# Kernel tuning notes

Hardware: AMD Instinct MI355X
Metric: run time of the kernel (lower is better)

## Reference

```python
import jax, jax.numpy as jnp
import numpy as np

D = 256; NH = 8; NL = 4; NP = 4; HD = D // NH
SHAPES = np.array([[180, 180], [90, 90], [45, 45], [23, 23]], dtype=np.int32)
LQ = int((SHAPES[:, 0] * SHAPES[:, 1]).sum())  # 43054
STARTS = np.concatenate([[0], np.cumsum(SHAPES[:, 0] * SHAPES[:, 1])[:-1]]).astype(np.int32)


def setup_inputs():
    ks = jax.random.split(jax.random.key(0), 16)
    s = 0.02
    p = lambda k, shp: jax.random.normal(k, shp, jnp.float32) * s
    return {
        "query": jax.random.normal(ks[0], (1, LQ, D), jnp.float32),
        "ref_points": jax.random.uniform(ks[1], (1, LQ, NL, 2), dtype=jnp.float32),
        "pos": jax.random.normal(ks[2], (1, LQ, D), jnp.float32),
        "input_spatial_shapes": jnp.asarray(SHAPES),
        "input_level_start_index": jnp.asarray(STARTS),
        "w_off": p(ks[3], (D, NH * NL * NP * 2)), "b_off": p(ks[4], (NH * NL * NP * 2,)),
        "w_attn": p(ks[5], (D, NH * NL * NP)), "b_attn": p(ks[6], (NH * NL * NP,)),
        "w_val": p(ks[7], (D, D)), "b_val": jnp.zeros((D,), jnp.float32),
        "w_out": p(ks[8], (D, D)), "b_out": jnp.zeros((D,), jnp.float32),
        "g1": jnp.ones((D,), jnp.float32), "beta1": jnp.zeros((D,), jnp.float32),
        "w1": p(ks[9], (D, D)), "b1": jnp.zeros((D,), jnp.float32),
        "w2": p(ks[10], (D, D)), "b2": jnp.zeros((D,), jnp.float32),
        "g2": jnp.ones((D,), jnp.float32), "beta2": jnp.zeros((D,), jnp.float32),
    }


def _ln(x, g, b):
    m = x.mean(-1, keepdims=True)
    v = ((x - m) ** 2).mean(-1, keepdims=True)
    return (x - m) * jax.lax.rsqrt(v + 1e-5) * g + b


def _sample_level(v, Hl, Wl, loc):
    # v: (B, Hl*Wl, NH, HD); loc: (B, Lq, NH, NP, 2) normalized to [0,1]
    # Bilinear sampling matching F.grid_sample(align_corners=False, padding_mode='zeros')
    B, _, nh, d = v.shape
    Lq, P = loc.shape[1], loc.shape[3]
    vb = jnp.transpose(v, (0, 2, 1, 3))  # (B, NH, HW, d)
    x = loc[..., 0] * Wl - 0.5
    y = loc[..., 1] * Hl - 0.5
    x0 = jnp.floor(x); y0 = jnp.floor(y)
    fx = x - x0; fy = y - y0
    out = jnp.zeros((B, nh, Lq, P, d), v.dtype)
    for dy in (0, 1):
        for dx in (0, 1):
            xi = x0 + dx; yi = y0 + dy
            w = (fx if dx else 1.0 - fx) * (fy if dy else 1.0 - fy)
            valid = (xi >= 0) & (xi < Wl) & (yi >= 0) & (yi < Hl)
            xc = jnp.clip(xi, 0, Wl - 1).astype(jnp.int32)
            yc = jnp.clip(yi, 0, Hl - 1).astype(jnp.int32)
            idx = jnp.transpose(yc * Wl + xc, (0, 2, 1, 3)).reshape(B, nh, Lq * P)
            g = jnp.take_along_axis(vb, idx[..., None], axis=2).reshape(B, nh, Lq, P, d)
            wt = jnp.transpose(jnp.where(valid, w, 0.0), (0, 2, 1, 3))
            out = out + g * wt[..., None]
    return out  # (B, NH, Lq, NP, HD)


def _layer(query, ref_points, pos, shp, sti, w_off, b_off, w_attn, b_attn, w_val, b_val,
           w_out, b_out, g1, beta1, w1, b1, w2, b2, g2, beta2):
    B, Lq, _ = query.shape
    q = query + pos  # with_pos_embed
    value = (query @ w_val + b_val).reshape(B, Lq, NH, HD)
    off = (q @ w_off + b_off).reshape(B, Lq, NH, NL, NP, 2)
    aw = jax.nn.softmax((q @ w_attn + b_attn).reshape(B, Lq, NH, NL * NP), axis=-1)
    aw = aw.reshape(B, Lq, NH, NL, NP)
    # offset_normalizer = [W_l, H_l]
    norm = jnp.asarray(shp[:, ::-1].copy(), jnp.float32)
    loc = ref_points[:, :, None, :, None, :] + off / norm[None, None, None, :, None, :]
    acc = jnp.zeros((B, NH, Lq, HD), query.dtype)
    for l in range(NL):
        Hl, Wl = int(shp[l, 0]), int(shp[l, 1])
        st = int(sti[l])
        sampled = _sample_level(value[:, st:st + Hl * Wl], Hl, Wl, loc[:, :, :, l])
        wl = jnp.transpose(aw[:, :, :, l], (0, 2, 1, 3))  # (B, NH, Lq, NP)
        acc = acc + (sampled * wl[..., None]).sum(axis=3)
    attn_out = acc.transpose(0, 2, 1, 3).reshape(B, Lq, D) @ w_out + b_out
    # residual + LayerNorm + FFN (dropout is identity in eval mode)
    x = _ln(query + attn_out, g1, beta1)
    ffn = jax.nn.relu(x @ w1 + b1) @ w2 + b2
    return _ln(x + ffn, g2, beta2)


def reference(query, ref_points, pos, input_spatial_shapes, input_level_start_index,
              w_off, b_off, w_attn, b_attn, w_val, b_val, w_out, b_out,
              g1, beta1, w1, b1, w2, b2, g2, beta2):
    shp = np.asarray(input_spatial_shapes)
    sti = np.asarray(input_level_start_index)
    return _layer(query, ref_points, pos, shp, sti, w_off, b_off, w_attn, b_attn,
                  w_val, b_val, w_out, b_out, g1, beta1, w1, b1, w2, b2, g2, beta2)
```

## Files before the change

### kernel.cpp

```cpp
#include <hip/hip_runtime.h>

typedef unsigned short u16;
typedef unsigned int u32;
typedef float f32x4 __attribute__((ext_vector_type(4)));
typedef short i16x8 __attribute__((ext_vector_type(8)));
typedef __bf16 bf16x8_t __attribute__((ext_vector_type(8)));

#define LQ 43054

__device__ __forceinline__ float bf2f(u16 u) {
  union { u32 i; float f; } v; v.i = ((u32)u) << 16; return v.f;
}
__device__ __forceinline__ u16 f2bf(float f) {
  u32 i = __float_as_uint(f);
  return (u16)((i + 0x7FFFu + ((i >> 16) & 1u)) >> 16);
}

template <typename T>
__device__ __forceinline__ auto mfma_try(T a, T b, f32x4 c, int)
    -> decltype(__builtin_amdgcn_mfma_f32_16x16x32_bf16(a, b, c, 0, 0, 0)) {
  return __builtin_amdgcn_mfma_f32_16x16x32_bf16(a, b, c, 0, 0, 0);
}
template <typename T>
__device__ __forceinline__ f32x4 mfma_try(T a, T b, f32x4 c, long) {
  return __builtin_amdgcn_mfma_f32_16x16x32_bf16(
      __builtin_bit_cast(bf16x8_t, a), __builtin_bit_cast(bf16x8_t, b), c, 0, 0, 0);
}
__device__ __forceinline__ f32x4 mfma_bf16(i16x8 a, i16x8 b, f32x4 c) {
  return mfma_try(a, b, c, 0);
}

__global__ void transpose_all_kernel(
    const float* __restrict__ w_off, const float* __restrict__ w_attn,
    const float* __restrict__ w_val, const float* __restrict__ w_out,
    const float* __restrict__ w1, const float* __restrict__ w2,
    u16* __restrict__ wT) {
  int b = blockIdx.x;
  const float* src; u16* dst; int N; int col;
  if (b < 256)       { src = w_off;  dst = wT;          N = 256; col = b; }
  else if (b < 384)  { src = w_attn; dst = wT + 65536;  N = 128; col = b - 256; }
  else if (b < 640)  { src = w_val;  dst = wT + 98304;  N = 256; col = b - 384; }
  else if (b < 896)  { src = w_out;  dst = wT + 163840; N = 256; col = b - 640; }
  else if (b < 1152) { src = w1;     dst = wT + 229376; N = 256; col = b - 896; }
  else               { src = w2;     dst = wT + 294912; N = 256; col = b - 1152; }
  dst[col * 256 + threadIdx.x] = f2bf(src[threadIdx.x * N + col]);
}

template <int AIN, int MODE, int NT>
__global__ __launch_bounds__(256) void gemm_kernel(
    const void* __restrict__ Av, const u16* __restrict__ Bt,
    const float* __restrict__ bias, void* __restrict__ out, int M) {
  constexpr int N = NT * 64;
  __shared__ uint4 As[2048];
  __shared__ uint4 Bs[2048];
  const int tid = threadIdx.x;
  const int w = tid >> 6, lane = tid & 63, quad = lane >> 4, l16 = lane & 15;
  const int r0 = blockIdx.x * 64;
  if constexpr (AIN == 2) {
    const u16* A = (const u16*)Av;
#pragma unroll
    for (int it = 0; it < 8; ++it) {
      int e = tid + it * 256;
      int row = e >> 5, c = e & 31;
      int gr = r0 + row;
      uint4 v = make_uint4(0u, 0u, 0u, 0u);
      if (gr < M) v = ((const uint4*)A)[gr * 32 + c];
      As[row * 32 + (c ^ (row & 7))] = v;
    }
  } else {
    const float* A = (const float*)Av;
#pragma unroll
    for (int it = 0; it < 16; ++it) {
      int e = tid + it * 256;
      int row = e >> 6, c4 = e & 63;
      int gr = r0 + row;
      float4 v = make_float4(0.f, 0.f, 0.f, 0.f);
      if (gr < M) v = ((const float4*)A)[gr * 64 + c4];
      uint2 pk;
      pk.x = (u32)f2bf(v.x) | ((u32)f2bf(v.y) << 16);
      pk.y = (u32)f2bf(v.z) | ((u32)f2bf(v.w) << 16);
      int c = c4 >> 1, hf = c4 & 1;
      ((uint2*)As)[((row * 32 + (c ^ (row & 7))) << 1) | hf] = pk;
    }
  }
  __syncthreads();
  const int arow = w * 16 + l16;
  i16x8 afr[8];
#pragma unroll
  for (int kk = 0; kk < 8; ++kk)
    afr[kk] = __builtin_bit_cast(i16x8, As[arow * 32 + (((kk << 2) + quad) ^ (arow & 7))]);
  for (int nt = 0; nt < NT; ++nt) {
    __syncthreads();
#pragma unroll
    for (int it = 0; it < 8; ++it) {
      int e = tid + it * 256;
      int row = e >> 5, c = e & 31;
      Bs[row * 32 + (c ^ (row & 7))] = ((const uint4*)Bt)[(nt * 64 + row) * 32 + c];
    }
    __syncthreads();
#pragma unroll
    for (int ct = 0; ct < 4; ++ct) {
      const int brow = ct * 16 + l16;
      f32x4 acc = {0.f, 0.f, 0.f, 0.f};
#pragma unroll
      for (int kk = 0; kk < 8; ++kk) {
        i16x8 bfr = __builtin_bit_cast(i16x8, Bs[brow * 32 + (((kk << 2) + quad) ^ (brow & 7))]);
        acc = mfma_bf16(afr[kk], bfr, acc);
      }
      int col = nt * 64 + ct * 16 + l16;
      float bv = bias[col];
#pragma unroll
      for (int r = 0; r < 4; ++r) {
        int grow = r0 + w * 16 + (quad << 2) + r;
        if (grow < M) {
          float val = acc[r] + bv;
          if (MODE == 1) ((u16*)out)[grow * N + col] = f2bf(val);
          else           ((u16*)out)[grow * N + col] = f2bf(fmaxf(val, 0.f));
        }
      }
    }
  }
}

__global__ __launch_bounds__(256) void offaw_gemm_kernel(
    const float* __restrict__ query, const float* __restrict__ pos,
    const u16* __restrict__ Bt, const float* __restrict__ b_off,
    const float* __restrict__ b_attn, u16* __restrict__ offb,
    float* __restrict__ aw, int M) {
  __shared__ uint4 As[2048];
  __shared__ uint4 Bs[2048];
  const int tid = threadIdx.x;
  const int w = tid >> 6, lane = tid & 63, quad = lane >> 4, l16 = lane & 15;
  const int r0 = blockIdx.x * 64;
#pragma unroll
  for (int it = 0; it < 16; ++it) {
    int e = tid + it * 256;
    int row = e >> 6, c4 = e & 63;
    int gr = r0 + row;
    float4 v = make_float4(0.f, 0.f, 0.f, 0.f);
    if (gr < M) {
      v = ((const float4*)query)[gr * 64 + c4];
      float4 p = ((const float4*)pos)[gr * 64 + c4];
      v.x += p.x; v.y += p.y; v.z += p.z; v.w += p.w;
    }
    uint2 pk;
    pk.x = (u32)f2bf(v.x) | ((u32)f2bf(v.y) << 16);
    pk.y = (u32)f2bf(v.z) | ((u32)f2bf(v.w) << 16);
    int c = c4 >> 1, hf = c4 & 1;
    ((uint2*)As)[((row * 32 + (c ^ (row & 7))) << 1) | hf] = pk;
  }
  __syncthreads();
  const int arow = w * 16 + l16;
  i16x8 afr[8];
#pragma unroll
  for (int kk = 0; kk < 8; ++kk)
    afr[kk] = __builtin_bit_cast(i16x8, As[arow * 32 + (((kk << 2) + quad) ^ (arow & 7))]);
  for (int nt = 0; nt < 6; ++nt) {
    __syncthreads();
#pragma unroll
    for (int it = 0; it < 8; ++it) {
      int e = tid + it * 256;
      int row = e >> 5, c = e & 31;
      Bs[row * 32 + (c ^ (row & 7))] = ((const uint4*)Bt)[(nt * 64 + row) * 32 + c];
    }
    __syncthreads();
#pragma unroll
    for (int ct = 0; ct < 4; ++ct) {
      const int brow = ct * 16 + l16;
      f32x4 acc = {0.f, 0.f, 0.f, 0.f};
#pragma unroll
      for (int kk = 0; kk < 8; ++kk) {
        i16x8 bfr = __builtin_bit_cast(i16x8, Bs[brow * 32 + (((kk << 2) + quad) ^ (brow & 7))]);
        acc = mfma_bf16(afr[kk], bfr, acc);
      }
      int colc = nt * 64 + ct * 16 + l16;
      if (nt < 4) {
        float bv = b_off[colc];
#pragma unroll
        for (int r = 0; r < 4; ++r) {
          int grow = r0 + w * 16 + (quad << 2) + r;
          if (grow < M) ((u16*)offb)[grow * 256 + colc] = f2bf(acc[r] + bv);
        }
      } else {
        float bv = b_attn[colc - 256];
#pragma unroll
        for (int r = 0; r < 4; ++r) {
          float v = acc[r] + bv;
          float m = v;
#pragma unroll
          for (int o = 1; o < 16; o <<= 1) m = fmaxf(m, __shfl_xor(m, o));
          float e = __expf(v - m);
          float s = e;
#pragma unroll
          for (int o = 1; o < 16; o <<= 1) s += __shfl_xor(s, o);
          int grow = r0 + w * 16 + (quad << 2) + r;
          if (grow < M) aw[grow * 128 + (colc - 256)] = e / s;
        }
      }
    }
  }
}

template <int RBF, int OBF>
__global__ __launch_bounds__(256) void gemm_ln_kernel(
    const u16* __restrict__ A, const u16* __restrict__ Bt,
    const float* __restrict__ bias, const void* __restrict__ residv,
    const float* __restrict__ g, const float* __restrict__ beta,
    void* __restrict__ outv, int M) {
  __shared__ uint4 As[2048];
  __shared__ uint4 Bs[2048];
  const int tid = threadIdx.x;
  const int w = tid >> 6, lane = tid & 63, quad = lane >> 4, l16 = lane & 15;
  const int r0 = blockIdx.x * 64;
#pragma unroll
  for (int it = 0; it < 8; ++it) {
    int e = tid + it * 256;
    int row = e >> 5, c = e & 31;
    int gr = r0 + row;
    uint4 v = make_uint4(0u, 0u, 0u, 0u);
    if (gr < M) v = ((const uint4*)A)[gr * 32 + c];
    As[row * 32 + (c ^ (row & 7))] = v;
  }
  __syncthreads();
  const int arow = w * 16 + l16;
  i16x8 afr[8];
#pragma unroll
  for (int kk = 0; kk < 8; ++kk)
    afr[kk] = __builtin_bit_cast(i16x8, As[arow * 32 + (((kk << 2) + quad) ^ (arow & 7))]);
  f32x4 acc[4][4];
#pragma unroll
  for (int nt = 0; nt < 4; ++nt)
#pragma unroll
    for (int ct = 0; ct < 4; ++ct) acc[nt][ct] = f32x4{0.f, 0.f, 0.f, 0.f};
  for (int nt = 0; nt < 4; ++nt) {
    __syncthreads();
#pragma unroll
    for (int it = 0; it < 8; ++it) {
      int e = tid + it * 256;
      int row = e >> 5, c = e & 31;
      Bs[row * 32 + (c ^ (row & 7))] = ((const uint4*)Bt)[(nt * 64 + row) * 32 + c];
    }
    __syncthreads();
#pragma unroll
    for (int ct = 0; ct < 4; ++ct) {
      const int brow = ct * 16 + l16;
#pragma unroll
      for (int kk = 0; kk < 8; ++kk) {
        i16x8 bfr = __builtin_bit_cast(i16x8, Bs[brow * 32 + (((kk << 2) + quad) ^ (brow & 7))]);
        acc[nt][ct] = mfma_bf16(afr[kk], bfr, acc[nt][ct]);
      }
    }
  }
  float breg[16], greg[16], bereg[16];
#pragma unroll
  for (int nt = 0; nt < 4; ++nt)
#pragma unroll
    for (int ct = 0; ct < 4; ++ct) {
      int col = nt * 64 + ct * 16 + l16;
      breg[nt * 4 + ct] = bias[col];
      greg[nt * 4 + ct] = g[col];
      bereg[nt * 4 + ct] = beta[col];
    }
  const int baserow = r0 + w * 16 + (quad << 2);
#pragma unroll
  for (int r = 0; r < 4; ++r) {
    int row = baserow + r;
    bool ok = row < M;
    float vals[16];
    float s = 0.f, s2 = 0.f;
#pragma unroll
    for (int nt = 0; nt < 4; ++nt)
#pragma unroll
      for (int ct = 0; ct < 4; ++ct) {
        int col = nt * 64 + ct * 16 + l16;
        float rv = 0.f;
        if (ok) rv = RBF ? bf2f(((const u16*)residv)[row * 256 + col])
                         : ((const float*)residv)[row * 256 + col];
        float val = acc[nt][ct][r] + breg[nt * 4 + ct] + rv;
        vals[nt * 4 + ct] = val;
        s += val; s2 += val * val;
      }
#pragma unroll
    for (int o = 1; o < 16; o <<= 1) { s += __shfl_xor(s, o); s2 += __shfl_xor(s2, o); }
    float m = s * (1.f / 256.f);
    float var = s2 * (1.f / 256.f) - m * m;
    float invs = rsqrtf(var + 1e-5f);
    if (ok) {
#pragma unroll
      for (int nt = 0; nt < 4; ++nt)
#pragma unroll
        for (int ct = 0; ct < 4; ++ct) {
          int col = nt * 64 + ct * 16 + l16;
          float o = (vals[nt * 4 + ct] - m) * invs * greg[nt * 4 + ct] + bereg[nt * 4 + ct];
          if (OBF) ((u16*)outv)[row * 256 + col] = f2bf(o);
          else     ((float*)outv)[row * 256 + col] = o;
        }
    }
  }
}

__global__ __launch_bounds__(256) void sampler_kernel(
    const float* __restrict__ refp,
    const u16* __restrict__ offb,
    const float* __restrict__ aw,
    const u16* __restrict__ value,
    u32* __restrict__ accv) {
  __shared__ uint4 rec[272];
  const int t = threadIdx.x;
  const int b = blockIdx.x;
  {
    const int qs = t >> 7, j = t & 127;
    const int i = b * 2 + qs;
    const int h = j >> 4, lp = j & 15, l = lp >> 2;
    const int Wl = (l == 0) ? 180 : (l == 1) ? 90 : (l == 2) ? 45 : 23;
    const int st = (l == 0) ? 0 : (l == 1) ? 32400 : (l == 2) ? 40500 : 42525;
    const float wj = aw[i * 128 + j];
    const u32 o2 = *(const u32*)(offb + i * 256 + h * 32 + lp * 2);
    const float ox = bf2f((u16)(o2 & 0xffffu)), oy = bf2f((u16)(o2 >> 16));
    const float rx = refp[i * 8 + l * 2], ry = refp[i * 8 + l * 2 + 1];
    float x = rx * (float)Wl + ox - 0.5f;
    float y = ry * (float)Wl + oy - 0.5f;
    float x0f = floorf(x), y0f = floorf(y);
    float fx = x - x0f, fy = y - y0f;
    int x0 = (int)x0f, y0 = (int)y0f;
    bool vx0 = (x0 >= 0) & (x0 < Wl), vx1 = (x0 + 1 >= 0) & (x0 + 1 < Wl);
    bool vy0 = (y0 >= 0) & (y0 < Wl), vy1 = (y0 + 1 >= 0) & (y0 + 1 < Wl);
    int x0c = min(max(x0, 0), Wl - 1), x1c = min(max(x0 + 1, 0), Wl - 1);
    int y0c = min(max(y0, 0), Wl - 1), y1c = min(max(y0 + 1, 0), Wl - 1);
    float w00 = (vx0 & vy0) ? wj * (1.f - fx) * (1.f - fy) : 0.f;
    float w01 = (vx1 & vy0) ? wj * fx * (1.f - fy) : 0.f;
    float w10 = (vx0 & vy1) ? wj * (1.f - fx) * fy : 0.f;
    float w11 = (vx1 & vy1) ? wj * fx * fy : 0.f;
    uint4 r;
    r.x = (u32)((st + y0c * Wl + x0c) * 512 + h * 64) | (u32)(x1c - x0c);
    r.y = (u32)(y1c - y0c) * (u32)(Wl * 512);
    r.z = (u32)f2bf(w00) | ((u32)f2bf(w01) << 16);
    r.w = (u32)f2bf(w10) | ((u32)f2bf(w11) << 16);
    rec[qs * 136 + h * 17 + lp] = r;
  }
  __syncthreads();
  const int qs = t >> 7, j = t & 127;
  const int h = j >> 4, dp = j & 15;
  const char* vb = (const char*)value;
  float a0 = 0.f, a1 = 0.f;
  const int rbase = qs * 136 + h * 17;
#pragma unroll
  for (int p = 0; p < 16; ++p) {
    uint4 r = rec[rbase + p];
    u32 base = (r.x & 0xFFFFFFFEu) + (u32)(dp * 4);
    u32 dxo = (r.x & 1u) << 9;
    u32 dyo = r.y;
    float w00 = __uint_as_float(r.z << 16);
    float w01 = __uint_as_float(r.z & 0xFFFF0000u);
    float w10 = __uint_as_float(r.w << 16);
    float w11 = __uint_as_float(r.w & 0xFFFF0000u);
    u32 p00 = *(const u32*)(vb + base);
    u32 p01 = *(const u32*)(vb + base + dxo);
    u32 p10 = *(const u32*)(vb + base + dyo);
    u32 p11 = *(const u32*)(vb + base + dyo + dxo);
    a0 = fmaf(w00, __uint_as_float(p00 << 16), a0);
    a1 = fmaf(w00, __uint_as_float(p00 & 0xFFFF0000u), a1);
    a0 = fmaf(w01, __uint_as_float(p01 << 16), a0);
    a1 = fmaf(w01, __uint_as_float(p01 & 0xFFFF0000u), a1);
    a0 = fmaf(w10, __uint_as_float(p10 << 16), a0);
    a1 = fmaf(w10, __uint_as_float(p10 & 0xFFFF0000u), a1);
    a0 = fmaf(w11, __uint_as_float(p11 << 16), a0);
    a1 = fmaf(w11, __uint_as_float(p11 & 0xFFFF0000u), a1);
  }
  u32 pk = (u32)f2bf(a0) | ((u32)f2bf(a1) << 16);
  accv[(b * 2 + qs) * 128 + j] = pk;
}

extern "C" void kernel_launch(void* const* d_in, const int* in_sizes, int n_in,
                              void* d_out, int out_size, void* d_ws, size_t ws_size,
                              hipStream_t stream) {
  const float* query  = (const float*)d_in[0];
  const float* refp   = (const float*)d_in[1];
  const float* pos    = (const float*)d_in[2];
  const float* w_off  = (const float*)d_in[5];
  const float* b_off  = (const float*)d_in[6];
  const float* w_attn = (const float*)d_in[7];
  const float* b_attn = (const float*)d_in[8];
  const float* w_val  = (const float*)d_in[9];
  const float* b_val  = (const float*)d_in[10];
  const float* w_out  = (const float*)d_in[11];
  const float* b_out  = (const float*)d_in[12];
  const float* g1     = (const float*)d_in[13];
  const float* beta1  = (const float*)d_in[14];
  const float* w1     = (const float*)d_in[15];
  const float* b1     = (const float*)d_in[16];
  const float* w2     = (const float*)d_in[17];
  const float* b2     = (const float*)d_in[18];
  const float* g2     = (const float*)d_in[19];
  const float* beta2  = (const float*)d_in[20];

  char* ws = (char*)d_ws;
  u16*   wT    = (u16*)(ws + 0);
  u16*   value = (u16*)(ws + 720896);
  u16*   offb  = (u16*)(ws + 22764544);
  float* aw    = (float*)(ws + 44808192);
  u16*   accb  = (u16*)(ws + 66851840);
  u16*   xb    = (u16*)(ws + 720896);
  u16*   hb    = (u16*)(ws + 22764544);

  u16* woffT  = wT;
  u16* wvalT  = wT + 98304;
  u16* woutT  = wT + 163840;
  u16* w1T    = wT + 229376;
  u16* w2T    = wT + 294912;

  transpose_all_kernel<<<1408, 256, 0, stream>>>(w_off, w_attn, w_val, w_out, w1, w2, wT);

  const int gm = (LQ + 63) / 64;
  gemm_kernel<0, 1, 4><<<gm, 256, 0, stream>>>(query, wvalT, b_val, value, LQ);
  offaw_gemm_kernel<<<gm, 256, 0, stream>>>(query, pos, woffT, b_off, b_attn, offb, aw, LQ);
  sampler_kernel<<<LQ / 2, 256, 0, stream>>>(refp, offb, aw, value, (u32*)accb);
  gemm_ln_kernel<0, 1><<<gm, 256, 0, stream>>>(accb, woutT, b_out, query, g1, beta1, xb, LQ);
  gemm_kernel<2, 2, 4><<<gm, 256, 0, stream>>>(xb, w1T, b1, hb, LQ);
  gemm_ln_kernel<1, 0><<<gm, 256, 0, stream>>>(hb, w2T, b2, xb, g2, beta2, d_out, LQ);
}
```

Baseline: 461.3 us.

## Load GEMM B fragments directly from global memory, dropping LDS staging

The GEMM kernels stop staging weight tiles in shared memory with per-tile barriers. Each wave now reads its B fragments straight from global (L2-cached) transposed weights into registers and runs the MFMAs on them. Shared memory per block is halved, and launch bounds are set so 3-4 blocks fit per CU. The cost is redundant global/L2 reads of the weights across waves and blocks, with uncoalesced 16-byte strided loads.

```diff
diff --git a/kernel.cpp b/kernel.cpp
--- a/kernel.cpp
+++ b/kernel.cpp
@@ -46,172 +46,7 @@
   dst[col * 256 + threadIdx.x] = f2bf(src[threadIdx.x * N + col]);
 }
 
-template <int AIN, int MODE, int NT>
-__global__ __launch_bounds__(256) void gemm_kernel(
-    const void* __restrict__ Av, const u16* __restrict__ Bt,
-    const float* __restrict__ bias, void* __restrict__ out, int M) {
-  constexpr int N = NT * 64;
-  __shared__ uint4 As[2048];
-  __shared__ uint4 Bs[2048];
-  const int tid = threadIdx.x;
-  const int w = tid >> 6, lane = tid & 63, quad = lane >> 4, l16 = lane & 15;
-  const int r0 = blockIdx.x * 64;
-  if constexpr (AIN == 2) {
-    const u16* A = (const u16*)Av;
-#pragma unroll
-    for (int it = 0; it < 8; ++it) {
-      int e = tid + it * 256;
-      int row = e >> 5, c = e & 31;
-      int gr = r0 + row;
-      uint4 v = make_uint4(0u, 0u, 0u, 0u);
-      if (gr < M) v = ((const uint4*)A)[gr * 32 + c];
-      As[row * 32 + (c ^ (row & 7))] = v;
-    }
-  } else {
-    const float* A = (const float*)Av;
-#pragma unroll
-    for (int it = 0; it < 16; ++it) {
-      int e = tid + it * 256;
-      int row = e >> 6, c4 = e & 63;
-      int gr = r0 + row;
-      float4 v = make_float4(0.f, 0.f, 0.f, 0.f);
-      if (gr < M) v = ((const float4*)A)[gr * 64 + c4];
-      uint2 pk;
-      pk.x = (u32)f2bf(v.x) | ((u32)f2bf(v.y) << 16);
-      pk.y = (u32)f2bf(v.z) | ((u32)f2bf(v.w) << 16);
-      int c = c4 >> 1, hf = c4 & 1;
-      ((uint2*)As)[((row * 32 + (c ^ (row & 7))) << 1) | hf] = pk;
-    }
-  }
-  __syncthreads();
-  const int arow = w * 16 + l16;
-  i16x8 afr[8];
-#pragma unroll
-  for (int kk = 0; kk < 8; ++kk)
-    afr[kk] = __builtin_bit_cast(i16x8, As[arow * 32 + (((kk << 2) + quad) ^ (arow & 7))]);
-  for (int nt = 0; nt < NT; ++nt) {
-    __syncthreads();
-#pragma unroll
-    for (int it = 0; it < 8; ++it) {
-      int e = tid + it * 256;
-      int row = e >> 5, c = e & 31;
-      Bs[row * 32 + (c ^ (row & 7))] = ((const uint4*)Bt)[(nt * 64 + row) * 32 + c];
-    }
-    __syncthreads();
-#pragma unroll
-    for (int ct = 0; ct < 4; ++ct) {
-      const int brow = ct * 16 + l16;
-      f32x4 acc = {0.f, 0.f, 0.f, 0.f};
-#pragma unroll
-      for (int kk = 0; kk < 8; ++kk) {
-        i16x8 bfr = __builtin_bit_cast(i16x8, Bs[brow * 32 + (((kk << 2) + quad) ^ (brow & 7))]);
-        acc = mfma_bf16(afr[kk], bfr, acc);
-      }
-      int col = nt * 64 + ct * 16 + l16;
-      float bv = bias[col];
-#pragma unroll
-      for (int r = 0; r < 4; ++r) {
-        int grow = r0 + w * 16 + (quad << 2) + r;
-        if (grow < M) {
-          float val = acc[r] + bv;
-          if (MODE == 1) ((u16*)out)[grow * N + col] = f2bf(val);
-          else           ((u16*)out)[grow * N + col] = f2bf(fmaxf(val, 0.f));
-        }
-      }
-    }
-  }
-}
-
-__global__ __launch_bounds__(256) void offaw_gemm_kernel(
-    const float* __restrict__ query, const float* __restrict__ pos,
-    const u16* __restrict__ Bt, const float* __restrict__ b_off,
-    const float* __restrict__ b_attn, u16* __restrict__ offb,
-    float* __restrict__ aw, int M) {
-  __shared__ uint4 As[2048];
-  __shared__ uint4 Bs[2048];
-  const int tid = threadIdx.x;
-  const int w = tid >> 6, lane = tid & 63, quad = lane >> 4, l16 = lane & 15;
-  const int r0 = blockIdx.x * 64;
-#pragma unroll
-  for (int it = 0; it < 16; ++it) {
-    int e = tid + it * 256;
-    int row = e >> 6, c4 = e & 63;
-    int gr = r0 + row;
-    float4 v = make_float4(0.f, 0.f, 0.f, 0.f);
-    if (gr < M) {
-      v = ((const float4*)query)[gr * 64 + c4];
-      float4 p = ((const float4*)pos)[gr * 64 + c4];
-      v.x += p.x; v.y += p.y; v.z += p.z; v.w += p.w;
-    }
-    uint2 pk;
-    pk.x = (u32)f2bf(v.x) | ((u32)f2bf(v.y) << 16);
-    pk.y = (u32)f2bf(v.z) | ((u32)f2bf(v.w) << 16);
-    int c = c4 >> 1, hf = c4 & 1;
-    ((uint2*)As)[((row * 32 + (c ^ (row & 7))) << 1) | hf] = pk;
-  }
-  __syncthreads();
-  const int arow = w * 16 + l16;
-  i16x8 afr[8];
-#pragma unroll
-  for (int kk = 0; kk < 8; ++kk)
-    afr[kk] = __builtin_bit_cast(i16x8, As[arow * 32 + (((kk << 2) + quad) ^ (arow & 7))]);
-  for (int nt = 0; nt < 6; ++nt) {
-    __syncthreads();
-#pragma unroll
-    for (int it = 0; it < 8; ++it) {
-      int e = tid + it * 256;
-      int row = e >> 5, c = e & 31;
-      Bs[row * 32 + (c ^ (row & 7))] = ((const uint4*)Bt)[(nt * 64 + row) * 32 + c];
-    }
-    __syncthreads();
-#pragma unroll
-    for (int ct = 0; ct < 4; ++ct) {
-      const int brow = ct * 16 + l16;
-      f32x4 acc = {0.f, 0.f, 0.f, 0.f};
-#pragma unroll
-      for (int kk = 0; kk < 8; ++kk) {
-        i16x8 bfr = __builtin_bit_cast(i16x8, Bs[brow * 32 + (((kk << 2) + quad) ^ (brow & 7))]);
-        acc = mfma_bf16(afr[kk], bfr, acc);
-      }
-      int colc = nt * 64 + ct * 16 + l16;
-      if (nt < 4) {
-        float bv = b_off[colc];
-#pragma unroll
-        for (int r = 0; r < 4; ++r) {
-          int grow = r0 + w * 16 + (quad << 2) + r;
-          if (grow < M) ((u16*)offb)[grow * 256 + colc] = f2bf(acc[r] + bv);
-        }
-      } else {
-        float bv = b_attn[colc - 256];
-#pragma unroll
-        for (int r = 0; r < 4; ++r) {
-          float v = acc[r] + bv;
-          float m = v;
-#pragma unroll
-          for (int o = 1; o < 16; o <<= 1) m = fmaxf(m, __shfl_xor(m, o));
-          float e = __expf(v - m);
-          float s = e;
-#pragma unroll
-          for (int o = 1; o < 16; o <<= 1) s += __shfl_xor(s, o);
-          int grow = r0 + w * 16 + (quad << 2) + r;
-          if (grow < M) aw[grow * 128 + (colc - 256)] = e / s;
-        }
-      }
-    }
-  }
-}
-
-template <int RBF, int OBF>
-__global__ __launch_bounds__(256) void gemm_ln_kernel(
-    const u16* __restrict__ A, const u16* __restrict__ Bt,
-    const float* __restrict__ bias, const void* __restrict__ residv,
-    const float* __restrict__ g, const float* __restrict__ beta,
-    void* __restrict__ outv, int M) {
-  __shared__ uint4 As[2048];
-  __shared__ uint4 Bs[2048];
-  const int tid = threadIdx.x;
-  const int w = tid >> 6, lane = tid & 63, quad = lane >> 4, l16 = lane & 15;
-  const int r0 = blockIdx.x * 64;
+__device__ __forceinline__ void stage_a_bf16(uint4* As, const u16* A, int r0, int M, int tid) {
 #pragma unroll
   for (int it = 0; it < 8; ++it) {
     int e = tid + it * 256;
@@ -221,80 +56,194 @@
     if (gr < M) v = ((const uint4*)A)[gr * 32 + c];
     As[row * 32 + (c ^ (row & 7))] = v;
   }
+}
+template <int ADD>
+__device__ __forceinline__ void stage_a_f32(uint4* As, const float* A, const float* A2,
+                                            int r0, int M, int tid) {
+#pragma unroll
+  for (int it = 0; it < 16; ++it) {
+    int e = tid + it * 256;
+    int row = e >> 6, c4 = e & 63;
+    int gr = r0 + row;
+    float4 v = make_float4(0.f, 0.f, 0.f, 0.f);
+    if (gr < M) {
+      v = ((const float4*)A)[gr * 64 + c4];
+      if constexpr (ADD) {
+        float4 p = ((const float4*)A2)[gr * 64 + c4];
+        v.x += p.x; v.y += p.y; v.z += p.z; v.w += p.w;
+      }
+    }
+    uint2 pk;
+    pk.x = (u32)f2bf(v.x) | ((u32)f2bf(v.y) << 16);
+    pk.y = (u32)f2bf(v.z) | ((u32)f2bf(v.w) << 16);
+    int c = c4 >> 1, hf = c4 & 1;
+    ((uint2*)As)[((row * 32 + (c ^ (row & 7))) << 1) | hf] = pk;
+  }
+}
+
+template <int AIN, int MODE, int NT>
+__global__ __launch_bounds__(256, 4) void gemm_kernel(
+    const void* __restrict__ Av, const u16* __restrict__ Bt,
+    const float* __restrict__ bias, void* __restrict__ out, int M) {
+  constexpr int N = NT * 64;
+  __shared__ uint4 As[2048];
+  const int tid = threadIdx.x;
+  const int w = tid >> 6, lane = tid & 63, quad = lane >> 4, l16 = lane & 15;
+  const int r0 = blockIdx.x * 64;
+  if constexpr (AIN == 2) stage_a_bf16(As, (const u16*)Av, r0, M, tid);
+  else                    stage_a_f32<0>(As, (const float*)Av, nullptr, r0, M, tid);
   __syncthreads();
   const int arow = w * 16 + l16;
   i16x8 afr[8];
 #pragma unroll
   for (int kk = 0; kk < 8; ++kk)
     afr[kk] = __builtin_bit_cast(i16x8, As[arow * 32 + (((kk << 2) + quad) ^ (arow & 7))]);
-  f32x4 acc[4][4];
-#pragma unroll
-  for (int nt = 0; nt < 4; ++nt)
-#pragma unroll
-    for (int ct = 0; ct < 4; ++ct) acc[nt][ct] = f32x4{0.f, 0.f, 0.f, 0.f};
-  for (int nt = 0; nt < 4; ++nt) {
-    __syncthreads();
-#pragma unroll
-    for (int it = 0; it < 8; ++it) {
-      int e = tid + it * 256;
-      int row = e >> 5, c = e & 31;
-      Bs[row * 32 + (c ^ (row & 7))] = ((const uint4*)Bt)[(nt * 64 + row) * 32 + c];
-    }
-    __syncthreads();
-#pragma unroll
-    for (int ct = 0; ct < 4; ++ct) {
-      const int brow = ct * 16 + l16;
-#pragma unroll
-      for (int kk = 0; kk < 8; ++kk) {
-        i16x8 bfr = __builtin_bit_cast(i16x8, Bs[brow * 32 + (((kk << 2) + quad) ^ (brow & 7))]);
-        acc[nt][ct] = mfma_bf16(afr[kk], bfr, acc[nt][ct]);
-      }
-    }
-  }
-  float breg[16], greg[16], bereg[16];
-#pragma unroll
-  for (int nt = 0; nt < 4; ++nt)
-#pragma unroll
-    for (int ct = 0; ct < 4; ++ct) {
-      int col = nt * 64 + ct * 16 + l16;
-      breg[nt * 4 + ct] = bias[col];
-      greg[nt * 4 + ct] = g[col];
-      bereg[nt * 4 + ct] = beta[col];
-    }
   const int baserow = r0 + w * 16 + (quad << 2);
 #pragma unroll
+  for (int t = 0; t < NT * 4; ++t) {
+    const uint4* bp = (const uint4*)Bt + (t * 16 + l16) * 32 + quad;
+    i16x8 bfr[8];
+#pragma unroll
+    for (int kk = 0; kk < 8; ++kk) bfr[kk] = __builtin_bit_cast(i16x8, bp[kk << 2]);
+    f32x4 acc = {0.f, 0.f, 0.f, 0.f};
+#pragma unroll
+    for (int kk = 0; kk < 8; ++kk) acc = mfma_bf16(afr[kk], bfr[kk], acc);
+    const int col = t * 16 + l16;
+    const float bv = bias[col];
+#pragma unroll
+    for (int r = 0; r < 4; ++r) {
+      int grow = baserow + r;
+      if (grow < M) {
+        float val = acc[r] + bv;
+        if (MODE == 1) ((u16*)out)[grow * N + col] = f2bf(val);
+        else           ((u16*)out)[grow * N + col] = f2bf(fmaxf(val, 0.f));
+      }
+    }
+  }
+}
+
+__global__ __launch_bounds__(256, 4) void offaw_gemm_kernel(
+    const float* __restrict__ query, const float* __restrict__ pos,
+    const u16* __restrict__ Bt, const float* __restrict__ b_off,
+    const float* __restrict__ b_attn, u16* __restrict__ offb,
+    float* __restrict__ aw, int M) {
+  __shared__ uint4 As[2048];
+  const int tid = threadIdx.x;
+  const int w = tid >> 6, lane = tid & 63, quad = lane >> 4, l16 = lane & 15;
+  const int r0 = blockIdx.x * 64;
+  stage_a_f32<1>(As, query, pos, r0, M, tid);
+  __syncthreads();
+  const int arow = w * 16 + l16;
+  i16x8 afr[8];
+#pragma unroll
+  for (int kk = 0; kk < 8; ++kk)
+    afr[kk] = __builtin_bit_cast(i16x8, As[arow * 32 + (((kk << 2) + quad) ^ (arow & 7))]);
+  const int baserow = r0 + w * 16 + (quad << 2);
+#pragma unroll
+  for (int t = 0; t < 24; ++t) {
+    const uint4* bp = (const uint4*)Bt + (t * 16 + l16) * 32 + quad;
+    i16x8 bfr[8];
+#pragma unroll
+    for (int kk = 0; kk < 8; ++kk) bfr[kk] = __builtin_bit_cast(i16x8, bp[kk << 2]);
+    f32x4 acc = {0.f, 0.f, 0.f, 0.f};
+#pragma unroll
+    for (int kk = 0; kk < 8; ++kk) acc = mfma_bf16(afr[kk], bfr[kk], acc);
+    if (t < 16) {
+      const int col = t * 16 + l16;
+      const float bv = b_off[col];
+#pragma unroll
+      for (int r = 0; r < 4; ++r) {
+        int grow = baserow + r;
+        if (grow < M) ((u16*)offb)[grow * 256 + col] = f2bf(acc[r] + bv);
+      }
+    } else {
+      const int colc = (t - 16) * 16 + l16;
+      const float bv = b_attn[colc];
+#pragma unroll
+      for (int r = 0; r < 4; ++r) {
+        float v = acc[r] + bv;
+        float m = v;
+#pragma unroll
+        for (int o = 1; o < 16; o <<= 1) m = fmaxf(m, __shfl_xor(m, o));
+        float e = __expf(v - m);
+        float s = e;
+#pragma unroll
+        for (int o = 1; o < 16; o <<= 1) s += __shfl_xor(s, o);
+        int grow = baserow + r;
+        if (grow < M) aw[grow * 128 + colc] = e / s;
+      }
+    }
+  }
+}
+
+template <int RBF, int OBF>
+__global__ __launch_bounds__(256, 3) void gemm_ln_kernel(
+    const u16* __restrict__ A, const u16* __restrict__ Bt,
+    const float* __restrict__ bias, const void* __restrict__ residv,
+    const float* __restrict__ g, const float* __restrict__ beta,
+    void* __restrict__ outv, int M) {
+  __shared__ uint4 As[2048];
+  const int tid = threadIdx.x;
+  const int w = tid >> 6, lane = tid & 63, quad = lane >> 4, l16 = lane & 15;
+  const int r0 = blockIdx.x * 64;
+  stage_a_bf16(As, A, r0, M, tid);
+  __syncthreads();
+  const int arow = w * 16 + l16;
+  i16x8 afr[8];
+#pragma unroll
+  for (int kk = 0; kk < 8; ++kk)
+    afr[kk] = __builtin_bit_cast(i16x8, As[arow * 32 + (((kk << 2) + quad) ^ (arow & 7))]);
+  const int baserow = r0 + w * 16 + (quad << 2);
+  f32x4 vals[16];
+  float s[4] = {0.f, 0.f, 0.f, 0.f}, s2[4] = {0.f, 0.f, 0.f, 0.f};
+#pragma unroll
+  for (int t = 0; t < 16; ++t) {
+    const uint4* bp = (const uint4*)Bt + (t * 16 + l16) * 32 + quad;
+    i16x8 bfr[8];
+#pragma unroll
+    for (int kk = 0; kk < 8; ++kk) bfr[kk] = __builtin_bit_cast(i16x8, bp[kk << 2]);
+    f32x4 acc = {0.f, 0.f, 0.f, 0.f};
+#pragma unroll
+    for (int kk = 0; kk < 8; ++kk) acc = mfma_bf16(afr[kk], bfr[kk], acc);
+    const int col = t * 16 + l16;
+    const float bv = bias[col];
+#pragma unroll
+    for (int r = 0; r < 4; ++r) {
+      int row = baserow + r;
+      float rv = 0.f;
+      if (row < M) rv = RBF ? bf2f(((const u16*)residv)[row * 256 + col])
+                            : ((const float*)residv)[row * 256 + col];
+      float val = acc[r] + bv + rv;
+      vals[t][r] = val;
+      s[r] += val; s2[r] += val * val;
+    }
+  }
+#pragma unroll
+  for (int r = 0; r < 4; ++r)
+#pragma unroll
+    for (int o = 1; o < 16; o <<= 1) {
+      s[r] += __shfl_xor(s[r], o);
+      s2[r] += __shfl_xor(s2[r], o);
+    }
+  float mr[4], ir[4];
+#pragma unroll
   for (int r = 0; r < 4; ++r) {
-    int row = baserow + r;
-    bool ok = row < M;
-    float vals[16];
-    float s = 0.f, s2 = 0.f;
-#pragma unroll
-    for (int nt = 0; nt < 4; ++nt)
-#pragma unroll
-      for (int ct = 0; ct < 4; ++ct) {
-        int col = nt * 64 + ct * 16 + l16;
-        float rv = 0.f;
-        if (ok) rv = RBF ? bf2f(((const u16*)residv)[row * 256 + col])
-                         : ((const float*)residv)[row * 256 + col];
-        float val = acc[nt][ct][r] + breg[nt * 4 + ct] + rv;
-        vals[nt * 4 + ct] = val;
-        s += val; s2 += val * val;
-      }
-#pragma unroll
-    for (int o = 1; o < 16; o <<= 1) { s += __shfl_xor(s, o); s2 += __shfl_xor(s2, o); }
-    float m = s * (1.f / 256.f);
-    float var = s2 * (1.f / 256.f) - m * m;
-    float invs = rsqrtf(var + 1e-5f);
-    if (ok) {
-#pragma unroll
-      for (int nt = 0; nt < 4; ++nt)
-#pragma unroll
-        for (int ct = 0; ct < 4; ++ct) {
-          int col = nt * 64 + ct * 16 + l16;
-          float o = (vals[nt * 4 + ct] - m) * invs * greg[nt * 4 + ct] + bereg[nt * 4 + ct];
-          if (OBF) ((u16*)outv)[row * 256 + col] = f2bf(o);
-          else     ((float*)outv)[row * 256 + col] = o;
-        }
+    mr[r] = s[r] * (1.f / 256.f);
+    float var = s2[r] * (1.f / 256.f) - mr[r] * mr[r];
+    ir[r] = rsqrtf(var + 1e-5f);
+  }
+#pragma unroll
+  for (int t = 0; t < 16; ++t) {
+    const int col = t * 16 + l16;
+    const float gv = g[col], bev = beta[col];
+#pragma unroll
+    for (int r = 0; r < 4; ++r) {
+      int row = baserow + r;
+      if (row < M) {
+        float o = (vals[t][r] - mr[r]) * ir[r] * gv + bev;
+        if (OBF) ((u16*)outv)[row * 256 + col] = f2bf(o);
+        else     ((float*)outv)[row * 256 + col] = o;
+      }
     }
   }
 }
```

New measurement: 566.9 us. +22.9%, slower.
